# Performance work log

Hardware: AMD Instinct MI355X
Metric: run time of the kernel (lower is better)

## Reference

```python
import jax, jax.numpy as jnp
import numpy as np

DELAY = 8  # init kwarg delay=8


def setup_inputs() -> dict:
    key = jax.random.key(0)
    k1, k2, k3, k4 = jax.random.split(key, 4)
    B, S, F = 64, 2048, 256
    H = 512               # hidden_features (= 2*hf)
    hf = H // 2
    Din = F + 2 + hf      # input_features + 2 (pos enc) + hf
    fn_input = jax.random.normal(k1, (B, S, F), jnp.float32)
    hidden_state = jax.random.normal(k2, (H,), jnp.float32)
    W0 = jax.random.normal(k3, (H, Din), jnp.float32) / np.sqrt(Din).astype(np.float32)
    W1 = jax.random.normal(k4, (H, Din), jnp.float32) / np.sqrt(Din).astype(np.float32)
    return {"fn_input": fn_input, "hidden_state": hidden_state, "W0": W0, "W1": W1}


def _calc(h, s, W):
    # mean-center over the BATCH dim (dim=0 in the torch code)
    out = h - h.mean(axis=0, keepdims=True)
    z = jnp.concatenate([out, s], axis=1) @ W.T      # [B, 2*hf]
    o0, o1 = jnp.split(z, 2, axis=1)
    return jnp.clip(o0, 0.0, 6.0) * jnp.tanh(o1)      # relu6 * tanh gate


def _forward_pass(h, s, W0, W1):
    h0, h1 = jnp.split(h, 2, axis=1)
    o1 = (h1 + _calc(h0, s, W0)) * 0.5                # outputs[1], i=0
    o0 = (h0 + _calc(o1, s, W1)) * 0.5                # outputs[0], i=1
    return jnp.concatenate([o0, o1], axis=1)


def reference(fn_input, hidden_state, W0, W1):
    B, S, F = fn_input.shape
    T = S + DELAY
    # pad with zero inputs for the delay steps
    x_ext = jnp.concatenate([fn_input, jnp.zeros((B, DELAY, F), fn_input.dtype)], axis=1)
    idx = jnp.arange(1, T + 1, dtype=fn_input.dtype)
    factor = jnp.asarray((T + 1) / 2.0, fn_input.dtype)
    pe = jnp.stack([idx, (idx - factor) / factor], axis=-1)  # [T, 2]
    h0 = jnp.broadcast_to(hidden_state[None, :], (B, hidden_state.shape[0]))

    def step(h, xs_t):
        x_t, pe_t = xs_t  # [B, F], [2]
        s = jnp.concatenate(
            [x_t, jnp.broadcast_to(pe_t[None, :], (x_t.shape[0], 2))], axis=1)
        return _forward_pass(h, s, W0, W1), None

    h, _ = jax.lax.scan(step, h0, (jnp.swapaxes(x_ext, 0, 1), pe))
    return h  # [B, 2*hf] (return_sequences=False)
```

## Files before the change

### kernel.cpp

```cpp
#include <hip/hip_runtime.h>


#define T_TOT 2056
#define S_SEQ 2048

typedef _Float16 f16x8 __attribute__((ext_vector_type(8)));
typedef float f32x4 __attribute__((ext_vector_type(4)));

__device__ unsigned long long g_st0[8192];
__device__ unsigned long long g_st1[8192];
__device__ unsigned long long g_pa0[1024];
__device__ unsigned long long g_pa1[1024];

__global__ void init_ws() {
  const int i = (int)blockIdx.x * 256 + (int)threadIdx.x;
  g_st0[i] = 0ull;
  g_st1[i] = 0ull;
  if (i < 1024) { g_pa0[i] = 0ull; g_pa1[i] = 0ull; }
}

#define AL(P) __hip_atomic_load((P), __ATOMIC_RELAXED, __HIP_MEMORY_SCOPE_AGENT)
#define AS(P, V)                                                               \
  __hip_atomic_store((P), (V), __ATOMIC_RELAXED, __HIP_MEMORY_SCOPE_AGENT)

#define PHASE(WS, SIN, PIN, TAGIN, SOUT, POUT, TAGOUT, RAW)                    \
  {                                                                            \
    const unsigned long long* pp_ = (PIN) + 4 * tid;                           \
    const unsigned long long* sp_ =                                            \
        (SIN) + (size_t)(16 * b + n) * 128 + (2 * wv) * 16 + kq * 4;           \
    unsigned long long q0_, q1_, q2_, q3_;                                     \
    unsigned long long s0_, s1_, s2_, s3_, s4_, s5_, s6_, s7_;                 \
    const unsigned tg_ = (unsigned)(TAGIN);                                    \
    int it_ = 0;                                                               \
    for (;;) {                                                                 \
      q0_ = AL(pp_ + 0); q1_ = AL(pp_ + 1);                                    \
      q2_ = AL(pp_ + 2); q3_ = AL(pp_ + 3);                                    \
      s0_ = AL(sp_ + 0); s1_ = AL(sp_ + 1);                                    \
      s2_ = AL(sp_ + 2); s3_ = AL(sp_ + 3);                                    \
      s4_ = AL(sp_ + 16); s5_ = AL(sp_ + 17);                                  \
      s6_ = AL(sp_ + 18); s7_ = AL(sp_ + 19);                                  \
      const unsigned ok_ =                                                     \
          ((unsigned)(q0_ >> 32) >= tg_) & ((unsigned)(q1_ >> 32) >= tg_) &    \
          ((unsigned)(q2_ >> 32) >= tg_) & ((unsigned)(q3_ >> 32) >= tg_) &    \
          ((unsigned)(s0_ >> 32) >= tg_) & ((unsigned)(s1_ >> 32) >= tg_) &    \
          ((unsigned)(s2_ >> 32) >= tg_) & ((unsigned)(s3_ >> 32) >= tg_) &    \
          ((unsigned)(s4_ >> 32) >= tg_) & ((unsigned)(s5_ >> 32) >= tg_) &    \
          ((unsigned)(s6_ >> 32) >= tg_) & ((unsigned)(s7_ >> 32) >= tg_);     \
      if (ok_) break;                                                          \
      if (!alive || ++it_ > (1 << 17)) { alive = 0; break; }                   \
    }                                                                          \
    const float mean_ = (__uint_as_float((unsigned)q0_) +                      \
                         __uint_as_float((unsigned)q1_) +                      \
                         __uint_as_float((unsigned)q2_) +                      \
                         __uint_as_float((unsigned)q3_)) * 0.015625f;          \
    mean_h[tid] = (_Float16)mean_;                                             \
    {                                                                          \
      unsigned long long* lp_ =                                                \
          (unsigned long long*)&lds_s[n][(2 * wv) * 16 + kq * 4];              \
      lp_[0] = ((unsigned long long)(unsigned)s1_ << 32) | (unsigned)s0_;      \
      lp_[1] = ((unsigned long long)(unsigned)s3_ << 32) | (unsigned)s2_;      \
      lp_[8] = ((unsigned long long)(unsigned)s5_ << 32) | (unsigned)s4_;      \
      lp_[9] = ((unsigned long long)(unsigned)s7_ << 32) | (unsigned)s6_;      \
    }                                                                          \
    __syncthreads();                                                           \
    _Pragma("unroll")                                                          \
    for (int kk = 0; kk < 8; ++kk) {                                           \
      const f16x8 sv_ = *(const f16x8*)&lds_s[n][kk * 16 + kq * 4];            \
      const f16x8 mv_ = *(const f16x8*)&mean_h[kk * 32 + kq * 8];              \
      if (kk & 1)                                                              \
        acc1 = __builtin_amdgcn_mfma_f32_16x16x32_f16(sv_ - mv_, (WS)[kk],     \
                                                      acc1, 0, 0, 0);          \
      else                                                                     \
        acc0 = __builtin_amdgcn_mfma_f32_16x16x32_f16(sv_ - mv_, (WS)[kk],     \
                                                      acc0, 0, 0, 0);          \
    }                                                                          \
    float nv_[4], ssum_ = 0.f;                                                 \
    _Pragma("unroll")                                                          \
    for (int r = 0; r < 4; ++r) {                                              \
      const float z = acc0[r] + acc1[r];                                       \
      const float p = __shfl_xor(z, 8);                                        \
      const float z0 = (n < 8) ? z : p;                                        \
      const float z1 = (n < 8) ? p : z;                                        \
       \
      const float z1c = fminf(fmaxf(z1, -10.f), 10.f);                         \
      const float e2 = __expf(2.f * z1c);                                      \
      const float th = (e2 - 1.f) * __builtin_amdgcn_rcpf(e2 + 1.f);           \
      const float cv = fminf(fmaxf(z0, 0.f), 6.f) * th;                        \
      const float o = ((RAW)[r] + cv) * 0.5f;                                  \
      (RAW)[r] = o; nv_[r] = o; ssum_ += o;                                    \
    }                                                                          \
    ssum_ += __shfl_xor(ssum_, 16);                                            \
    ssum_ += __shfl_xor(ssum_, 32);                                            \
    _Pragma("unroll")                                                          \
    for (int r = 0; r < 4; ++r) {                                              \
      union { _Float16 h; unsigned short u; } hb_;                             \
      hb_.h = (_Float16)nv_[r];                                                \
      const unsigned pr_ = (unsigned)__shfl_xor((int)hb_.u, 1) & 0xFFFFu;      \
      if ((n & 1) == 0 && n < 8) {                                             \
        const unsigned dw_ = (unsigned)hb_.u | (pr_ << 16);                    \
        AS((SOUT) + (size_t)(16 * b + kq * 4 + r) * 128 + (ocol >> 1),         \
           ((unsigned long long)(unsigned)(TAGOUT) << 32) |                    \
               (unsigned long long)dw_);                                       \
      }                                                                        \
    }                                                                          \
    if (kq == 0 && n < 8)                                                      \
      AS((POUT) + (size_t)ocol * 4 + b,                                        \
         ((unsigned long long)(unsigned)(TAGOUT) << 32) |                      \
             (unsigned long long)__float_as_uint(ssum_));                      \
    __syncthreads();        \
  }

__launch_bounds__(256, 1)
__global__ void rnn_kernel(const float* __restrict__ xg,
                           const float* __restrict__ hs,
                           const float* __restrict__ W0,
                           const float* __restrict__ W1,
                           float* __restrict__ out) {
  const int wgid = (int)blockIdx.x;
  const int b = wgid & 3;
  const int c = wgid >> 2;
  const int tid = (int)threadIdx.x;
  const int wv = tid >> 6;
  const int ln = tid & 63;
  const int n = ln & 15;
  const int kq = ln >> 4;
  const int ocol = c * 32 + wv * 8 + (n & 7);
  const int wrow = (n < 8) ? ocol : (256 + ocol);

  __shared__ __align__(16) unsigned lds_s[16][132];
  __shared__ __align__(16) _Float16 mean_h[256];

  f16x8 w0s[8], w0x[8], w1s[8], w1x[8];
  float w0pa, w0pb, w1pa, w1pb;
  {
    const float* r0 = W0 + (size_t)wrow * 514;
    const float* r1 = W1 + (size_t)wrow * 514;
#pragma unroll
    for (int kk = 0; kk < 8; ++kk) {
      const int k0 = kk * 32 + kq * 8;
      f16x8 a, bx, a1, bx1;
#pragma unroll
      for (int j = 0; j < 8; ++j) {
        a[j]   = (_Float16)r0[k0 + j];
        bx[j]  = (_Float16)r0[256 + k0 + j];
        a1[j]  = (_Float16)r1[k0 + j];
        bx1[j] = (_Float16)r1[256 + k0 + j];
      }
      w0s[kk] = a; w0x[kk] = bx; w1s[kk] = a1; w1x[kk] = bx1;
    }
    w0pa = r0[512]; w0pb = r0[513];
    w1pa = r1[512]; w1pb = r1[513];
  }

  float raw0[4], raw1[4];
#pragma unroll
  for (int r = 0; r < 4; ++r) { raw0[r] = hs[ocol]; raw1[r] = hs[256 + ocol]; }

  int alive = 1;

  {
    union { _Float16 h; unsigned short u; } e0, e1;
    e0.h = (_Float16)hs[ocol]; e1.h = (_Float16)hs[ocol + 1];
    const unsigned dw = (unsigned)e0.u | ((unsigned)e1.u << 16);
    if ((n & 1) == 0 && n < 8) {
#pragma unroll
      for (int r = 0; r < 4; ++r)
        AS(g_st0 + (size_t)(16 * b + kq * 4 + r) * 128 + (ocol >> 1),
           (1ull << 32) | (unsigned long long)dw);
    }
    if (kq == 0 && n < 8)
      AS(g_pa0 + (size_t)ocol * 4 + b,
         (1ull << 32) |
             (unsigned long long)__float_as_uint(16.f * hs[ocol]));
  }

  f32x4 xf[16];
  f16x8 xa[8];
  const int arow = 16 * b + n;
  {
    const float* xp = xg + (size_t)arow * S_SEQ * 256 + kq * 8;
#pragma unroll
    for (int kk = 0; kk < 8; ++kk) {
      xf[2 * kk]     = *(const f32x4*)(xp + kk * 32);
      xf[2 * kk + 1] = *(const f32x4*)(xp + kk * 32 + 4);
    }
  }

  for (int t = 0; t < T_TOT; ++t) {
    const float pe0 = (float)(t + 1);
    const float pe1 = (pe0 - 1028.5f) * (1.0f / 1028.5f);
    const int have_x = (t < S_SEQ);

    {
      f32x4 acc0, acc1;
      const float pt = pe0 * w0pa + pe1 * w0pb;
      acc0[0] = pt; acc0[1] = pt; acc0[2] = pt; acc0[3] = pt;
      acc1[0] = 0.f; acc1[1] = 0.f; acc1[2] = 0.f; acc1[3] = 0.f;
      if (have_x) {
#pragma unroll
        for (int kk = 0; kk < 8; ++kk) {
          f16x8 af;
#pragma unroll
          for (int j = 0; j < 4; ++j) {
            af[j]     = (_Float16)xf[2 * kk][j];
            af[4 + j] = (_Float16)xf[2 * kk + 1][j];
          }
          xa[kk] = af;
          if (kk & 1)
            acc1 = __builtin_amdgcn_mfma_f32_16x16x32_f16(af, w0x[kk], acc1,
                                                          0, 0, 0);
          else
            acc0 = __builtin_amdgcn_mfma_f32_16x16x32_f16(af, w0x[kk], acc0,
                                                          0, 0, 0);
        }
      }
      PHASE(w0s, g_st0, g_pa0, 2 * t + 1, g_st1, g_pa1, 2 * t + 2, raw1);
    }

    {
      f32x4 acc0, acc1;
      const float pt = pe0 * w1pa + pe1 * w1pb;
      acc0[0] = pt; acc0[1] = pt; acc0[2] = pt; acc0[3] = pt;
      acc1[0] = 0.f; acc1[1] = 0.f; acc1[2] = 0.f; acc1[3] = 0.f;
      if (have_x) {
#pragma unroll
        for (int kk = 0; kk < 8; ++kk) {
          if (kk & 1)
            acc1 = __builtin_amdgcn_mfma_f32_16x16x32_f16(xa[kk], w1x[kk],
                                                          acc1, 0, 0, 0);
          else
            acc0 = __builtin_amdgcn_mfma_f32_16x16x32_f16(xa[kk], w1x[kk],
                                                          acc0, 0, 0, 0);
        }
      }
      if (t + 1 < S_SEQ) {
        const float* xp = xg + ((size_t)arow * S_SEQ + (t + 1)) * 256 + kq * 8;
#pragma unroll
        for (int kk = 0; kk < 8; ++kk) {
          xf[2 * kk]     = *(const f32x4*)(xp + kk * 32);
          xf[2 * kk + 1] = *(const f32x4*)(xp + kk * 32 + 4);
        }
      }
      PHASE(w1s, g_st1, g_pa1, 2 * t + 2, g_st0, g_pa0, 2 * t + 3, raw0);
    }
  }

  if (n < 8) {
#pragma unroll
    for (int r = 0; r < 4; ++r) {
      const int row = 16 * b + kq * 4 + r;
      out[(size_t)row * 512 + ocol] = raw0[r];
      out[(size_t)row * 512 + 256 + ocol] = raw1[r];
    }
  }
}

#undef PHASE
#undef AS
#undef AL

extern "C" void kernel_launch(void* const* d_in, const int* in_sizes, int n_in,
                              void* d_out, int out_size, void* d_ws, size_t ws_size,
                              hipStream_t stream) {
  (void)in_sizes; (void)n_in; (void)out_size; (void)d_ws; (void)ws_size;
  const float* x  = (const float*)d_in[0];
  const float* hs = (const float*)d_in[1];
  const float* W0 = (const float*)d_in[2];
  const float* W1 = (const float*)d_in[3];
  float* out = (float*)d_out;

  init_ws<<<dim3(32), dim3(256), 0, stream>>>();
  rnn_kernel<<<dim3(32), dim3(256), 0, stream>>>(x, hs, W0, W1, out);
}
```

Baseline: 14.76 ms.

## Merge column groups into fewer 512-thread blocks with local state and selective polling

The persistent RNN kernel goes from 32 blocks of 256 threads to 16 blocks of 512 threads, so each block owns 64 output columns. The block's own half of the hidden state is written straight into LDS double buffers, and only the three peer quarters are fetched from global memory. The spin-wait now re-polls only flags that are not yet ready, and fewer blocks means less cross-block handshaking on each of the 4112 serial phases. In exchange, each block does twice the MFMA work per phase, adds an extra __syncthreads for the mean reduction, and recomputes the f16 x conversion instead of keeping it in registers.

Measured after the change: 30.89 ms. 2.09x slower.

```diff
diff --git a/kernel.cpp b/kernel.cpp
--- a/kernel.cpp
+++ b/kernel.cpp
@@ -22,50 +22,44 @@
 #define AL(P) __hip_atomic_load((P), __ATOMIC_RELAXED, __HIP_MEMORY_SCOPE_AGENT)
 #define AS(P, V)                                                               \
   __hip_atomic_store((P), (V), __ATOMIC_RELAXED, __HIP_MEMORY_SCOPE_AGENT)
-
-#define PHASE(WS, SIN, PIN, TAGIN, SOUT, POUT, TAGOUT, RAW)                    \
+#define TOK(Q) ((unsigned)((Q) >> 32) >= tg_)
+
+#define PHASE(WS, HIN, HOUT, SIN, PIN, TAGIN, SOUT, POUT, TAGOUT, RAW)         \
   {                                                                            \
-    const unsigned long long* pp_ = (PIN) + 4 * tid;                           \
-    const unsigned long long* sp_ =                                            \
-        (SIN) + (size_t)(16 * b + n) * 128 + (2 * wv) * 16 + kq * 4;           \
-    unsigned long long q0_, q1_, q2_, q3_;                                     \
-    unsigned long long s0_, s1_, s2_, s3_, s4_, s5_, s6_, s7_;                 \
     const unsigned tg_ = (unsigned)(TAGIN);                                    \
+    const unsigned long long* mp_ =                                            \
+        (PIN) + 4 * (tid & 255) + 2 * (tid >> 8);                              \
+    const unsigned long long* sa_ = (SIN) + (size_t)(b * 4 + qa) * 512 + tid;  \
+    const unsigned long long* sb_ = (SIN) + (size_t)(b * 4 + qb) * 512 + tid;  \
+    const unsigned long long* sc_ = (SIN) + (size_t)(b * 4 + qc) * 512 + tid;  \
+    unsigned long long m0_ = AL(mp_), m1_ = AL(mp_ + 1);                       \
+    unsigned long long s0_ = AL(sa_), s1_ = AL(sb_), s2_ = AL(sc_);            \
     int it_ = 0;                                                               \
     for (;;) {                                                                 \
-      q0_ = AL(pp_ + 0); q1_ = AL(pp_ + 1);                                    \
-      q2_ = AL(pp_ + 2); q3_ = AL(pp_ + 3);                                    \
-      s0_ = AL(sp_ + 0); s1_ = AL(sp_ + 1);                                    \
-      s2_ = AL(sp_ + 2); s3_ = AL(sp_ + 3);                                    \
-      s4_ = AL(sp_ + 16); s5_ = AL(sp_ + 17);                                  \
-      s6_ = AL(sp_ + 18); s7_ = AL(sp_ + 19);                                  \
-      const unsigned ok_ =                                                     \
-          ((unsigned)(q0_ >> 32) >= tg_) & ((unsigned)(q1_ >> 32) >= tg_) &    \
-          ((unsigned)(q2_ >> 32) >= tg_) & ((unsigned)(q3_ >> 32) >= tg_) &    \
-          ((unsigned)(s0_ >> 32) >= tg_) & ((unsigned)(s1_ >> 32) >= tg_) &    \
-          ((unsigned)(s2_ >> 32) >= tg_) & ((unsigned)(s3_ >> 32) >= tg_) &    \
-          ((unsigned)(s4_ >> 32) >= tg_) & ((unsigned)(s5_ >> 32) >= tg_) &    \
-          ((unsigned)(s6_ >> 32) >= tg_) & ((unsigned)(s7_ >> 32) >= tg_);     \
-      if (ok_) break;                                                          \
-      if (!alive || ++it_ > (1 << 17)) { alive = 0; break; }                   \
-    }                                                                          \
-    const float mean_ = (__uint_as_float((unsigned)q0_) +                      \
-                         __uint_as_float((unsigned)q1_) +                      \
-                         __uint_as_float((unsigned)q2_) +                      \
-                         __uint_as_float((unsigned)q3_)) * 0.015625f;          \
-    mean_h[tid] = (_Float16)mean_;                                             \
+      if (TOK(m0_) && TOK(m1_) && TOK(s0_) && TOK(s1_) && TOK(s2_)) break;     \
+      if (!alive || ++it_ > (1 << 16)) { alive = 0; break; }                   \
+      if (!TOK(m0_)) m0_ = AL(mp_);                                            \
+      if (!TOK(m1_)) m1_ = AL(mp_ + 1);                                        \
+      if (!TOK(s0_)) s0_ = AL(sa_);                                            \
+      if (!TOK(s1_)) s1_ = AL(sb_);                                            \
+      if (!TOK(s2_)) s2_ = AL(sc_);                                            \
+    }                                                                          \
+    ps[tid >> 8][tid & 255] =                                                  \
+        __uint_as_float((unsigned)m0_) + __uint_as_float((unsigned)m1_);       \
     {                                                                          \
-      unsigned long long* lp_ =                                                \
-          (unsigned long long*)&lds_s[n][(2 * wv) * 16 + kq * 4];              \
-      lp_[0] = ((unsigned long long)(unsigned)s1_ << 32) | (unsigned)s0_;      \
-      lp_[1] = ((unsigned long long)(unsigned)s3_ << 32) | (unsigned)s2_;      \
-      lp_[8] = ((unsigned long long)(unsigned)s5_ << 32) | (unsigned)s4_;      \
-      lp_[9] = ((unsigned long long)(unsigned)s7_ << 32) | (unsigned)s6_;      \
-    }                                                                          \
+      const int r_ = tid >> 5, p_ = tid & 31;                                  \
+      HIN[r_][32 * qa + p_] = (unsigned)s0_;                                   \
+      HIN[r_][32 * qb + p_] = (unsigned)s1_;                                   \
+      HIN[r_][32 * qc + p_] = (unsigned)s2_;                                   \
+    }                                                                          \
+    __syncthreads();                                                           \
+    if (tid < 256)                                                             \
+      mean_h[tid] = (_Float16)((ps[0][tid] + ps[1][tid]) * 0.015625f);         \
     __syncthreads();                                                           \
     _Pragma("unroll")                                                          \
     for (int kk = 0; kk < 8; ++kk) {                                           \
-      const f16x8 sv_ = *(const f16x8*)&lds_s[n][kk * 16 + kq * 4];            \
+      const f16x8 sv_ = *(const f16x8*)((const _Float16*)&HIN[0][0] +          \
+                                        n * 272 + kk * 32 + kq * 8);           \
       const f16x8 mv_ = *(const f16x8*)&mean_h[kk * 32 + kq * 8];              \
       if (kk & 1)                                                              \
         acc1 = __builtin_amdgcn_mfma_f32_16x16x32_f16(sv_ - mv_, (WS)[kk],     \
@@ -98,19 +92,20 @@
       const unsigned pr_ = (unsigned)__shfl_xor((int)hb_.u, 1) & 0xFFFFu;      \
       if ((n & 1) == 0 && n < 8) {                                             \
         const unsigned dw_ = (unsigned)hb_.u | (pr_ << 16);                    \
-        AS((SOUT) + (size_t)(16 * b + kq * 4 + r) * 128 + (ocol >> 1),         \
+        HOUT[kq * 4 + r][32 * q + 4 * w + (n >> 1)] = dw_;                     \
+        AS((SOUT) + (size_t)(b * 4 + q) * 512 + (kq * 4 + r) * 32 + 4 * w +    \
+               (n >> 1),                                                       \
            ((unsigned long long)(unsigned)(TAGOUT) << 32) |                    \
                (unsigned long long)dw_);                                       \
       }                                                                        \
     }                                                                          \
     if (kq == 0 && n < 8)                                                      \
-      AS((POUT) + (size_t)ocol * 4 + b,                                        \
+      AS((POUT) + (size_t)ocg * 4 + b,                                         \
          ((unsigned long long)(unsigned)(TAGOUT) << 32) |                      \
              (unsigned long long)__float_as_uint(ssum_));                      \
-    __syncthreads();        \
-  }
-
-__launch_bounds__(256, 1)
+  }
+
+__launch_bounds__(512)
 __global__ void rnn_kernel(const float* __restrict__ xg,
                            const float* __restrict__ hs,
                            const float* __restrict__ W0,
@@ -118,16 +113,19 @@
                            float* __restrict__ out) {
   const int wgid = (int)blockIdx.x;
   const int b = wgid & 3;
-  const int c = wgid >> 2;
+  const int q = wgid >> 2;
+  const int qa = (q + 1) & 3, qb = (q + 2) & 3, qc = (q + 3) & 3;
   const int tid = (int)threadIdx.x;
-  const int wv = tid >> 6;
+  const int w = tid >> 6;
   const int ln = tid & 63;
   const int n = ln & 15;
   const int kq = ln >> 4;
-  const int ocol = c * 32 + wv * 8 + (n & 7);
-  const int wrow = (n < 8) ? ocol : (256 + ocol);
-
-  __shared__ __align__(16) unsigned lds_s[16][132];
+  const int ocg = 64 * q + 8 * w + (n & 7);
+  const int wrow = (n < 8) ? ocg : (256 + ocg);
+
+  __shared__ __align__(16) unsigned h0u[16][136];
+  __shared__ __align__(16) unsigned h1u[16][136];
+  __shared__ float ps[2][256];
   __shared__ __align__(16) _Float16 mean_h[256];
 
   f16x8 w0s[8], w0x[8], w1s[8], w1x[8];
@@ -154,28 +152,36 @@
 
   float raw0[4], raw1[4];
 #pragma unroll
-  for (int r = 0; r < 4; ++r) { raw0[r] = hs[ocol]; raw1[r] = hs[256 + ocol]; }
+  for (int r = 0; r < 4; ++r) { raw0[r] = hs[ocg]; raw1[r] = hs[256 + ocg]; }
 
   int alive = 1;
 
+#pragma unroll
+  for (int i = 0; i < 4; ++i) {
+    const int rc = tid + 512 * i;
+    const int r_ = rc >> 7, cp_ = rc & 127;
+    union { _Float16 h; unsigned short u; } e0, e1;
+    e0.h = (_Float16)hs[2 * cp_]; e1.h = (_Float16)hs[2 * cp_ + 1];
+    h0u[r_][cp_] = (unsigned)e0.u | ((unsigned)e1.u << 16);
+  }
+
   {
+    const int r_ = tid >> 5, p_ = tid & 31;
+    const int col = 64 * q + 2 * p_;
     union { _Float16 h; unsigned short u; } e0, e1;
-    e0.h = (_Float16)hs[ocol]; e1.h = (_Float16)hs[ocol + 1];
+    e0.h = (_Float16)hs[col]; e1.h = (_Float16)hs[col + 1];
     const unsigned dw = (unsigned)e0.u | ((unsigned)e1.u << 16);
-    if ((n & 1) == 0 && n < 8) {
-#pragma unroll
-      for (int r = 0; r < 4; ++r)
-        AS(g_st0 + (size_t)(16 * b + kq * 4 + r) * 128 + (ocol >> 1),
-           (1ull << 32) | (unsigned long long)dw);
-    }
-    if (kq == 0 && n < 8)
-      AS(g_pa0 + (size_t)ocol * 4 + b,
-         (1ull << 32) |
-             (unsigned long long)__float_as_uint(16.f * hs[ocol]));
-  }
+    AS(g_st0 + (size_t)(b * 4 + q) * 512 + r_ * 32 + p_,
+       (1ull << 32) | (unsigned long long)dw);
+    if (tid < 64) {
+      const int c_ = 64 * q + tid;
+      AS(g_pa0 + (size_t)c_ * 4 + b,
+         (1ull << 32) | (unsigned long long)__float_as_uint(16.f * hs[c_]));
+    }
+  }
+  __syncthreads();
 
   f32x4 xf[16];
-  f16x8 xa[8];
   const int arow = 16 * b + n;
   {
     const float* xp = xg + (size_t)arow * S_SEQ * 256 + kq * 8;
@@ -205,7 +211,6 @@
             af[j]     = (_Float16)xf[2 * kk][j];
             af[4 + j] = (_Float16)xf[2 * kk + 1][j];
           }
-          xa[kk] = af;
           if (kk & 1)
             acc1 = __builtin_amdgcn_mfma_f32_16x16x32_f16(af, w0x[kk], acc1,
                                                           0, 0, 0);
@@ -214,7 +219,8 @@
                                                           0, 0, 0);
         }
       }
-      PHASE(w0s, g_st0, g_pa0, 2 * t + 1, g_st1, g_pa1, 2 * t + 2, raw1);
+      PHASE(w0s, h0u, h1u, g_st0, g_pa0, 2 * t + 1, g_st1, g_pa1, 2 * t + 2,
+            raw1);
     }
 
     {
@@ -225,12 +231,18 @@
       if (have_x) {
 #pragma unroll
         for (int kk = 0; kk < 8; ++kk) {
+          f16x8 af;
+#pragma unroll
+          for (int j = 0; j < 4; ++j) {
+            af[j]     = (_Float16)xf[2 * kk][j];
+            af[4 + j] = (_Float16)xf[2 * kk + 1][j];
+          }
           if (kk & 1)
-            acc1 = __builtin_amdgcn_mfma_f32_16x16x32_f16(xa[kk], w1x[kk],
-                                                          acc1, 0, 0, 0);
+            acc1 = __builtin_amdgcn_mfma_f32_16x16x32_f16(af, w1x[kk], acc1,
+                                                          0, 0, 0);
           else
-            acc0 = __builtin_amdgcn_mfma_f32_16x16x32_f16(xa[kk], w1x[kk],
-                                                          acc0, 0, 0, 0);
+            acc0 = __builtin_amdgcn_mfma_f32_16x16x32_f16(af, w1x[kk], acc0,
+                                                          0, 0, 0);
         }
       }
       if (t + 1 < S_SEQ) {
@@ -241,7 +253,8 @@
           xf[2 * kk + 1] = *(const f32x4*)(xp + kk * 32 + 4);
         }
       }
-      PHASE(w1s, g_st1, g_pa1, 2 * t + 2, g_st0, g_pa0, 2 * t + 3, raw0);
+      PHASE(w1s, h1u, h0u, g_st1, g_pa1, 2 * t + 2, g_st0, g_pa0, 2 * t + 3,
+            raw0);
     }
   }
 
@@ -249,13 +262,14 @@
 #pragma unroll
     for (int r = 0; r < 4; ++r) {
       const int row = 16 * b + kq * 4 + r;
-      out[(size_t)row * 512 + ocol] = raw0[r];
-      out[(size_t)row * 512 + 256 + ocol] = raw1[r];
+      out[(size_t)row * 512 + ocg] = raw0[r];
+      out[(size_t)row * 512 + 256 + ocg] = raw1[r];
     }
   }
 }
 
 #undef PHASE
+#undef TOK
 #undef AS
 #undef AL
 
@@ -270,5 +284,5 @@
   float* out = (float*)d_out;
 
   init_ws<<<dim3(32), dim3(256), 0, stream>>>();
-  rnn_kernel<<<dim3(32), dim3(256), 0, stream>>>(x, hs, W0, W1, out);
+  rnn_kernel<<<dim3(16), dim3(512), 0, stream>>>(x, hs, W0, W1, out);
 }
```
